# Kernel optimization log

Hardware: AMD Instinct MI355X
Metric: run time of the kernel (lower is better)

## Reference

```python
import jax, jax.numpy as jnp
import numpy as np

B, S, D = 4, 4096, 256
H, K = 4, 64  # num_heads, key_dim
EPS = 1e-3    # Keras LayerNormalization default epsilon
NEG = -1e9    # Keras additive mask constant for float32


def setup_inputs() -> dict:
    key = jax.random.key(0)
    ks = jax.random.split(key, 12)
    sd = 1.0 / np.sqrt(D)
    return {
        "query": jax.random.normal(ks[0], (B, S, D), dtype=jnp.float32),
        "value": jax.random.normal(ks[1], (B, S, D), dtype=jnp.float32),
        "Wq": jax.random.normal(ks[2], (D, H, K), dtype=jnp.float32) * sd,
        "bq": jnp.zeros((H, K), dtype=jnp.float32),
        "Wk": jax.random.normal(ks[3], (D, H, K), dtype=jnp.float32) * sd,
        "bk": jnp.zeros((H, K), dtype=jnp.float32),
        "Wv": jax.random.normal(ks[4], (D, H, K), dtype=jnp.float32) * sd,
        "bv": jnp.zeros((H, K), dtype=jnp.float32),
        "Wo": jax.random.normal(ks[5], (H, K, D), dtype=jnp.float32) * sd,
        "bo": jnp.zeros((D,), dtype=jnp.float32),
        "gamma": jnp.ones((D,), dtype=jnp.float32),
        "beta": jnp.zeros((D,), dtype=jnp.float32),
    }


def reference(query, value, Wq, bq, Wk, bk, Wv, bv, Wo, bo, gamma, beta):
    # Keras MHA(query, value): key defaults to value
    q = jnp.einsum("bsd,dhk->bshk", query, Wq) + bq
    k = jnp.einsum("bsd,dhk->bshk", value, Wk) + bk
    v = jnp.einsum("bsd,dhk->bshk", value, Wv) + bv
    scores = jnp.einsum("bqhk,bshk->bhqs", q, k) / jnp.sqrt(jnp.float32(K))
    # lower-triangular causal mask, applied additively (Keras semantics)
    causal = jnp.tril(jnp.ones((q.shape[1], q.shape[1]), dtype=bool))
    scores = scores + jnp.where(causal, 0.0, NEG)
    attn = jax.nn.softmax(scores, axis=-1)  # [B,H,S,S]
    ctx = jnp.einsum("bhqs,bshk->bqhk", attn, v)
    mha_out = jnp.einsum("bqhk,hkd->bqd", ctx, Wo) + bo
    # residual + LayerNorm (over last axis)
    x = mha_out + query
    mu = jnp.mean(x, axis=-1, keepdims=True)
    var = jnp.mean(jnp.square(x - mu), axis=-1, keepdims=True)
    return (x - mu) * jax.lax.rsqrt(var + EPS) * gamma + beta
```

## Files before the change

kernel.cpp:

```cpp
#include <hip/hip_runtime.h>
#include <hip/hip_bf16.h>
#include <stdint.h>

#define SS 4096
#define DD 256
#define HH 4
#define KK 64
#define ALPHA 0.18033688011112042f

typedef float f32x4 __attribute__((ext_vector_type(4)));
typedef short s16x8 __attribute__((ext_vector_type(8)));
typedef unsigned int u32;

__device__ __forceinline__ unsigned short f2bf(float x) {
  union { float f; unsigned u; } v; v.f = x;
  unsigned r = v.u + 0x7fffu + ((v.u >> 16) & 1u);
  return (unsigned short)(r >> 16);
}

__device__ __forceinline__ u32 cvtpk(float lo, float hi) {
  u32 r;
  asm("v_cvt_pk_bf16_f32 %0, %1, %2" : "=v"(r) : "v"(lo), "v"(hi));
  return r;
}

#define fexp2(x) __builtin_amdgcn_exp2f(x)

__device__ __forceinline__ void gl_lds16(const unsigned short* g, unsigned short* l) {
  __builtin_amdgcn_global_load_lds(
      (const __attribute__((address_space(1))) u32*)g,
      (__attribute__((address_space(3))) u32*)l, 16, 0, 0);
}

__global__ void wprep(const float* __restrict__ Wq, const float* __restrict__ Wk,
                      const float* __restrict__ Wv, const float* __restrict__ Wo,
                      unsigned short* __restrict__ Wt, unsigned short* __restrict__ Wot)
{
  const int blk = blockIdx.x, t = threadIdx.x;
  const int rsub = t >> 4;
  const int c0 = (t & 15) * 16;
  if (blk < 48) {
    const int n = blk * 16 + rsub;
    const float* W = (n < 256) ? Wq : ((n < 512) ? Wk : Wv);
    const int nn = n & 255;
    const float sc = (n < 256) ? ALPHA : 1.0f;
    for (int c = c0; c < c0 + 16; ++c)
      Wt[(size_t)n * 256 + c] = f2bf(sc * W[(size_t)c * 256 + nn]);
  } else {
    const int d = (blk - 48) * 16 + rsub;
    for (int c = c0; c < c0 + 16; ++c)
      Wot[(size_t)d * 256 + c] = f2bf(Wo[(size_t)c * 256 + d]);
  }
}

__global__ __launch_bounds__(256, 3) void qkv_mfma(
    const float* __restrict__ query, const float* __restrict__ value,
    const unsigned short* __restrict__ Wt,
    const float* __restrict__ bq, const float* __restrict__ bk,
    const float* __restrict__ bv,
    unsigned short* __restrict__ qb, unsigned short* __restrict__ kbs,
    unsigned short* __restrict__ vts)
{
  __shared__ __align__(16) unsigned short Xs[64 * 256];

  const int t = threadIdx.x;
  const int w = t >> 6, l = t & 63, lr = l & 15, grp = l >> 4;
  const int mat = (int)(blockIdx.x % 3u);
  const int rb  = (int)(blockIdx.x / 3u);
  const long r0 = (long)rb * 64;

  const float* X = (mat == 0) ? query : value;

  {
    const int row = t >> 2;
    const int c0s = (t & 3) * 64;
    const float* xp = X + (r0 + row) * 256 + c0s;
    const int sw = (row & 7) << 3;
    #pragma unroll
    for (int g = 0; g < 8; ++g) {
      f32x4 x0 = *(const f32x4*)(xp + g * 8);
      f32x4 x1 = *(const f32x4*)(xp + g * 8 + 4);
      union { u32 wd[4]; s16x8 v; } bb;
      bb.wd[0] = cvtpk(x0[0], x0[1]);
      bb.wd[1] = cvtpk(x0[2], x0[3]);
      bb.wd[2] = cvtpk(x1[0], x1[1]);
      bb.wd[3] = cvtpk(x1[2], x1[3]);
      *(s16x8*)&Xs[(row * 256 + c0s + g * 8) ^ sw] = bb.v;
    }
  }
  __syncthreads();

  const int n0 = w * 64;
  const int swr = (lr & 7) << 3;

  f32x4 acc[4][4] = {};

  #pragma unroll 2
  for (int k0 = 0; k0 < 256; k0 += 32) {
    s16x8 xf[4];
    #pragma unroll
    for (int mt = 0; mt < 4; ++mt)
      xf[mt] = *(const s16x8*)&Xs[((mt * 16 + lr) * 256 + k0 + grp * 8) ^ swr];
    #pragma unroll
    for (int nt = 0; nt < 4; ++nt) {
      s16x8 af = *(const s16x8*)(Wt + (size_t)(mat * 256 + n0 + nt * 16 + lr) * 256 + k0 + grp * 8);
      if (mat == 2) {
        #pragma unroll
        for (int mt = 0; mt < 4; ++mt)
          acc[mt][nt] = __builtin_amdgcn_mfma_f32_16x16x32_bf16(xf[mt], af, acc[mt][nt], 0, 0, 0);
      } else {
        #pragma unroll
        for (int mt = 0; mt < 4; ++mt)
          acc[mt][nt] = __builtin_amdgcn_mfma_f32_16x16x32_bf16(af, xf[mt], acc[mt][nt], 0, 0, 0);
      }
    }
  }

  const int b  = (int)(r0 >> 12);
  const int s0 = (int)(r0 & 4095);
  const int kt = s0 >> 6;
  const size_t base = (size_t)(b * 4 + w) * (SS * KK) + (size_t)kt * 4096;

  if (mat == 0) {
    #pragma unroll
    for (int nt = 0; nt < 4; ++nt) {
      const int nk = nt * 16 + grp * 4;
      f32x4 bias = *(const f32x4*)&bq[n0 + nk] * ALPHA;
      #pragma unroll
      for (int mt = 0; mt < 4; ++mt) {
        const int s = s0 + mt * 16 + lr;
        f32x4 o = acc[mt][nt] + bias;
        uint2 pk2; pk2.x = cvtpk(o[0], o[1]); pk2.y = cvtpk(o[2], o[3]);
        *(uint2*)&qb[((size_t)(b * 4 + w) * SS + s) * KK + nk] = pk2;
      }
    }
  } else if (mat == 1) {
    #pragma unroll
    for (int nt = 0; nt < 4; ++nt) {
      const int d0 = nt * 16 + grp * 4;
      const int cc = d0 >> 5, grpk = (d0 >> 3) & 3, jlo = d0 & 7;
      f32x4 bias = *(const f32x4*)&bk[n0 + d0];
      #pragma unroll
      for (int mt = 0; mt < 4; ++mt) {
        const int chunk = ((mt * 2 + cc) * 4 + grpk) * 16 + lr;
        f32x4 o = acc[mt][nt] + bias;
        uint2 pk2; pk2.x = cvtpk(o[0], o[1]); pk2.y = cvtpk(o[2], o[3]);
        *(uint2*)&kbs[base + chunk * 8 + jlo] = pk2;
      }
    }
  } else {
    #pragma unroll
    for (int nt = 0; nt < 4; ++nt) {
      const float bvn = bv[n0 + nt * 16 + lr];
      #pragma unroll
      for (int mt = 0; mt < 4; ++mt) {
        const int cb = (nt * 2 + (mt >> 1)) * 64 + grp * 16 + lr;
        f32x4 o = acc[mt][nt] + bvn;
        uint2 pk2; pk2.x = cvtpk(o[0], o[1]); pk2.y = cvtpk(o[2], o[3]);
        *(uint2*)&vts[base + (size_t)cb * 8 + (mt & 1) * 4] = pk2;
      }
    }
  }
}

__global__ __launch_bounds__(256, 2) void attn(
    const unsigned short* __restrict__ qb,
    const unsigned short* __restrict__ kbs,
    const unsigned short* __restrict__ vts,
    float* __restrict__ num0, float* __restrict__ num1,
    float* __restrict__ lb0, float* __restrict__ lb1)
{
  __shared__ __align__(16) unsigned short Kl[2][4096];
  __shared__ __align__(16) unsigned short Vl[2][4096];

  const int t = threadIdx.x;
  const int w = t >> 6, l = t & 63, lr = l & 15, grp = l >> 4;

  const int i    = blockIdx.x;
  const int bh   = i & 15;
  const int pr   = (i >> 4) & 15;
  const int role = i >> 8;
  const int b = bh >> 2, h = bh & 3;
  const int phA_last = 2 * pr + 1;

  const unsigned short* kbase = kbs + (size_t)bh * (SS * KK);
  const unsigned short* vbase = vts + (size_t)bh * (SS * KK);
  const unsigned short* qpb   = qb  + (size_t)bh * (SS * KK);

  int sup = (role == 0) ? pr : (31 - pr);

  s16x8 qf[2][2];
  #pragma unroll
  for (int q2 = 0; q2 < 2; ++q2) {
    const unsigned short* qp = qpb + (size_t)(sup * 128 + w * 32 + q2 * 16 + lr) * KK;
    qf[q2][0] = *(const s16x8*)(qp + grp * 8);
    qf[q2][1] = *(const s16x8*)(qp + 32 + grp * 8);
  }

  s16x8 ones;
  #pragma unroll
  for (int e = 0; e < 8; ++e) ones[e] = (short)0x3F80;
  const f32x4 minit = {-16.f, -16.f, -16.f, -16.f};

  f32x4 cacc[2][4] = {};
  f32x4 lacc[2] = {};

  const int off0 = (w * 64 + l) * 8;
  const int off1 = ((4 + w) * 64 + l) * 8;

  {
    const int kt0 = (role == 0) ? 0 : (31 - 2 * pr);
    const unsigned short* ks = kbase + (size_t)kt0 * 4096;
    const unsigned short* vs = vbase + (size_t)kt0 * 4096;
    gl_lds16(ks + off0, &Kl[0][w * 512]);
    gl_lds16(ks + off1, &Kl[0][(4 + w) * 512]);
    gl_lds16(vs + off0, &Vl[0][w * 512]);
    gl_lds16(vs + off1, &Vl[0][(4 + w) * 512]);
  }
  __syncthreads();

  for (int ss = 0; ss <= 32; ++ss) {
    const int cur = ss & 1;
    const int kt = (role == 0)
        ? ((ss <= phA_last) ? ss : (ss - (phA_last + 1)))
        : (31 - 2 * pr + ss);

    if (ss < 32) {
      const int ktn = (role == 0)
          ? ((ss + 1 <= phA_last) ? (ss + 1) : (ss + 1 - (phA_last + 1)))
          : (31 - 2 * pr + ss + 1);
      const unsigned short* ks = kbase + (size_t)ktn * 4096;
      const unsigned short* vs = vbase + (size_t)ktn * 4096;
      unsigned short* Kd = &Kl[cur ^ 1][0];
      unsigned short* Vd = &Vl[cur ^ 1][0];
      gl_lds16(ks + off0, Kd + w * 512);
      gl_lds16(ks + off1, Kd + (4 + w) * 512);
      gl_lds16(vs + off0, Vd + w * 512);
      gl_lds16(vs + off1, Vd + (4 + w) * 512);
    }

    if (!(kt == 2 * sup + 1 && w < 2)) {
      const unsigned short* Kb = &Kl[cur][0];
      const unsigned short* Vb = &Vl[cur][0];

      s16x8 kf[8];
      #pragma unroll
      for (int kc = 0; kc < 8; ++kc)
        kf[kc] = *(const s16x8*)&Kb[((kc * 4 + grp) * 16 + lr) * 8];

      f32x4 sc[2][4];
      #pragma unroll
      for (int q2 = 0; q2 < 2; ++q2) {
        #pragma unroll
        for (int kvt = 0; kvt < 4; ++kvt) {
          f32x4 a = __builtin_amdgcn_mfma_f32_16x16x32_bf16(kf[kvt * 2 + 0], qf[q2][0], minit, 0, 0, 0);
          a = __builtin_amdgcn_mfma_f32_16x16x32_bf16(kf[kvt * 2 + 1], qf[q2][1], a, 0, 0, 0);
          sc[q2][kvt] = a;
        }
      }

      if (kt >= 2 * sup) {
        const int kvb0 = kt * 64;
        #pragma unroll
        for (int q2 = 0; q2 < 2; ++q2) {
          const int qrow = sup * 128 + w * 32 + q2 * 16 + lr;
          #pragma unroll
          for (int kvt = 0; kvt < 4; ++kvt)
            #pragma unroll
            for (int e = 0; e < 4; ++e)
              if ((kvb0 + kvt * 16 + grp * 4 + e) > qrow) sc[q2][kvt][e] += -1.0e9f;
        }
      }

      #pragma unroll
      for (int q2 = 0; q2 < 2; ++q2)
        #pragma unroll
        for (int kvt = 0; kvt < 4; ++kvt)
          #pragma unroll
          for (int e = 0; e < 4; ++e)
            sc[q2][kvt][e] = fexp2(sc[q2][kvt][e]);

      s16x8 pf[2][2];
      #pragma unroll
      for (int q2 = 0; q2 < 2; ++q2) {
        #pragma unroll
        for (int kap = 0; kap < 2; ++kap) {
          union { u32 wd[4]; s16x8 v; } pu;
          pu.wd[0] = cvtpk(sc[q2][2 * kap][0], sc[q2][2 * kap][1]);
          pu.wd[1] = cvtpk(sc[q2][2 * kap][2], sc[q2][2 * kap][3]);
          pu.wd[2] = cvtpk(sc[q2][2 * kap + 1][0], sc[q2][2 * kap + 1][1]);
          pu.wd[3] = cvtpk(sc[q2][2 * kap + 1][2], sc[q2][2 * kap + 1][3]);
          pf[q2][kap] = pu.v;
        }
      }

      #pragma unroll
      for (int m2 = 0; m2 < 4; ++m2) {
        #pragma unroll
        for (int kap = 0; kap < 2; ++kap) {
          s16x8 vfr = *(const s16x8*)&Vb[((m2 * 2 + kap) * 64 + l) * 8];
          cacc[0][m2] = __builtin_amdgcn_mfma_f32_16x16x32_bf16(vfr, pf[0][kap], cacc[0][m2], 0, 0, 0);
          cacc[1][m2] = __builtin_amdgcn_mfma_f32_16x16x32_bf16(vfr, pf[1][kap], cacc[1][m2], 0, 0, 0);
        }
      }
      #pragma unroll
      for (int q2 = 0; q2 < 2; ++q2) {
        lacc[q2] = __builtin_amdgcn_mfma_f32_16x16x32_bf16(ones, pf[q2][0], lacc[q2], 0, 0, 0);
        lacc[q2] = __builtin_amdgcn_mfma_f32_16x16x32_bf16(ones, pf[q2][1], lacc[q2], 0, 0, 0);
      }
    }

    if (role == 0 && ss == phA_last) {
      #pragma unroll
      for (int q2 = 0; q2 < 2; ++q2) {
        const int rowg = sup * 128 + w * 32 + q2 * 16 + lr;
        float* np_ = num0 + ((size_t)((b << 12) + rowg)) * 256 + h * 64;
        #pragma unroll
        for (int m2 = 0; m2 < 4; ++m2) {
          *(f32x4*)&np_[m2 * 16 + grp * 4] = cacc[q2][m2];
          cacc[q2][m2] = (f32x4){0.f, 0.f, 0.f, 0.f};
        }
        if (grp == 0) lb0[(bh << 12) + rowg] = lacc[q2][0];
        lacc[q2] = (f32x4){0.f, 0.f, 0.f, 0.f};
      }
      sup = 31 - pr;
      #pragma unroll
      for (int q2 = 0; q2 < 2; ++q2) {
        const unsigned short* qp = qpb + (size_t)(sup * 128 + w * 32 + q2 * 16 + lr) * KK;
        qf[q2][0] = *(const s16x8*)(qp + grp * 8);
        qf[q2][1] = *(const s16x8*)(qp + 32 + grp * 8);
      }
    }
    __syncthreads();
  }

  if (role == 0) {
    #pragma unroll
    for (int q2 = 0; q2 < 2; ++q2) {
      const int rowg = sup * 128 + w * 32 + q2 * 16 + lr;
      float* np_ = num0 + ((size_t)((b << 12) + rowg)) * 256 + h * 64;
      #pragma unroll
      for (int m2 = 0; m2 < 4; ++m2)
        *(f32x4*)&np_[m2 * 16 + grp * 4] = cacc[q2][m2];
      if (grp == 0) lb0[(bh << 12) + rowg] = lacc[q2][0];
    }
  } else {
    #pragma unroll
    for (int q2 = 0; q2 < 2; ++q2) {
      const int rowg = sup * 128 + w * 32 + q2 * 16 + lr;
      float* np_ = num1 + ((size_t)((b << 11) + (rowg - 2048))) * 256 + h * 64;
      #pragma unroll
      for (int m2 = 0; m2 < 4; ++m2)
        *(f32x4*)&np_[m2 * 16 + grp * 4] = cacc[q2][m2];
      if (grp == 0) lb1[(bh << 11) + (rowg - 2048)] = lacc[q2][0];
    }
  }
}

__global__ __launch_bounds__(256, 4) void oproj_ln(
    const float* __restrict__ num0, const float* __restrict__ num1,
    const float* __restrict__ lb0, const float* __restrict__ lb1,
    const unsigned short* __restrict__ Wot,
    const float* __restrict__ bo, const float* __restrict__ query,
    const float* __restrict__ gamma, const float* __restrict__ beta,
    float* __restrict__ out)
{
  __shared__ __align__(16) float redS[32][4];
  __shared__ __align__(16) float redQ[32][4];

  const int t = threadIdx.x;
  const int w = t >> 6, l = t & 63, lr = l & 15, grp = l >> 4;
  const long r0 = (long)blockIdx.x * 32;
  const int n0c = w * 64;
  const int b = (int)(r0 >> 12);
  const bool heavy = ((r0 >> 11) & 1) != 0;

  float invl[2][4];
  #pragma unroll
  for (int mt = 0; mt < 2; ++mt) {
    const int grow = (int)r0 + mt * 16 + lr;
    #pragma unroll
    for (int h = 0; h < 4; ++h) {
      float lv = lb0[((b * 4 + h) << 12) + (grow & 4095)];
      if (heavy) lv += lb1[((b * 4 + h) << 11) + (grow & 2047)];
      invl[mt][h] = 1.0f / lv;
    }
  }

  f32x4 acc[2][4] = {};

  #pragma unroll
  for (int k0 = 0; k0 < 256; k0 += 32) {
    s16x8 bfr[2];
    #pragma unroll
    for (int mt = 0; mt < 2; ++mt) {
      const int grow = (int)r0 + mt * 16 + lr;
      const int c = k0 + grp * 8;
      const float* p0 = num0 + (size_t)grow * 256 + c;
      f32x4 a0 = *(const f32x4*)p0;
      f32x4 a1 = *(const f32x4*)(p0 + 4);
      if (heavy) {
        const float* p1 = num1 + ((size_t)((b << 11) + (grow & 2047))) * 256 + c;
        a0 += *(const f32x4*)p1;
        a1 += *(const f32x4*)(p1 + 4);
      }
      const float iv = invl[mt][k0 >> 6];
      a0 *= iv; a1 *= iv;
      union { u32 wd[4]; s16x8 v; } bb;
      bb.wd[0] = cvtpk(a0[0], a0[1]);
      bb.wd[1] = cvtpk(a0[2], a0[3]);
      bb.wd[2] = cvtpk(a1[0], a1[1]);
      bb.wd[3] = cvtpk(a1[2], a1[3]);
      bfr[mt] = bb.v;
    }
    #pragma unroll
    for (int nt = 0; nt < 4; ++nt) {
      s16x8 af = *(const s16x8*)(Wot + (size_t)(n0c + nt * 16 + lr) * 256 + k0 + grp * 8);
      acc[0][nt] = __builtin_amdgcn_mfma_f32_16x16x32_bf16(af, bfr[0], acc[0][nt], 0, 0, 0);
      acc[1][nt] = __builtin_amdgcn_mfma_f32_16x16x32_bf16(af, bfr[1], acc[1][nt], 0, 0, 0);
    }
  }

  float sm[2] = {0.f, 0.f}, sq[2] = {0.f, 0.f};
  #pragma unroll
  for (int mt = 0; mt < 2; ++mt) {
    const long s = r0 + mt * 16 + lr;
    #pragma unroll
    for (int nt = 0; nt < 4; ++nt) {
      const int n = n0c + nt * 16 + grp * 4;
      f32x4 v = acc[mt][nt] + *(const f32x4*)&bo[n] + *(const f32x4*)&query[s * 256 + n];
      acc[mt][nt] = v;
      sm[mt] += v[0] + v[1] + v[2] + v[3];
      sq[mt] += v[0]*v[0] + v[1]*v[1] + v[2]*v[2] + v[3]*v[3];
    }
    sm[mt] += __shfl_xor(sm[mt], 16); sm[mt] += __shfl_xor(sm[mt], 32);
    sq[mt] += __shfl_xor(sq[mt], 16); sq[mt] += __shfl_xor(sq[mt], 32);
  }
  if (grp == 0) {
    redS[0 * 16 + lr][w] = sm[0]; redQ[0 * 16 + lr][w] = sq[0];
    redS[1 * 16 + lr][w] = sm[1]; redQ[1 * 16 + lr][w] = sq[1];
  }
  __syncthreads();

  #pragma unroll
  for (int mt = 0; mt < 2; ++mt) {
    f32x4 s4 = *(const f32x4*)&redS[mt * 16 + lr][0];
    f32x4 q4 = *(const f32x4*)&redQ[mt * 16 + lr][0];
    const float tot = s4[0] + s4[1] + s4[2] + s4[3];
    const float tq  = q4[0] + q4[1] + q4[2] + q4[3];
    const float mu  = tot * 0.00390625f;
    const float var = tq * 0.00390625f - mu * mu;
    const float rs  = rsqrtf(var + 1.0e-3f);
    const long s = r0 + mt * 16 + lr;
    #pragma unroll
    for (int nt = 0; nt < 4; ++nt) {
      const int n = n0c + nt * 16 + grp * 4;
      f32x4 g = *(const f32x4*)&gamma[n];
      f32x4 bt = *(const f32x4*)&beta[n];
      f32x4 o = (acc[mt][nt] - mu) * rs * g + bt;
      *(f32x4*)&out[s * 256 + n] = o;
    }
  }
}

extern "C" void kernel_launch(void* const* d_in, const int* in_sizes, int n_in,
                              void* d_out, int out_size, void* d_ws, size_t ws_size,
                              hipStream_t stream) {
  const float* query = (const float*)d_in[0];
  const float* value = (const float*)d_in[1];
  const float* Wq    = (const float*)d_in[2];
  const float* bq    = (const float*)d_in[3];
  const float* Wk    = (const float*)d_in[4];
  const float* bk    = (const float*)d_in[5];
  const float* Wv    = (const float*)d_in[6];
  const float* bv    = (const float*)d_in[7];
  const float* Wo    = (const float*)d_in[8];
  const float* bo    = (const float*)d_in[9];
  const float* gamma = (const float*)d_in[10];
  const float* beta  = (const float*)d_in[11];
  float* out = (float*)d_out;

  char* ws = (char*)d_ws;
  unsigned short* qb   = (unsigned short*)ws;
  unsigned short* kbs  = (unsigned short*)(ws + ((size_t)8  << 20));
  unsigned short* vts  = (unsigned short*)(ws + ((size_t)16 << 20));
  float* num0          = (float*)(ws + ((size_t)24 << 20));
  float* num1          = (float*)(ws + ((size_t)40 << 20));
  float* lb0           = (float*)(ws + ((size_t)48 << 20));
  float* lb1           = (float*)(ws + ((size_t)48 << 20) + ((size_t)256 << 10));
  unsigned short* Wt   = (unsigned short*)(ws + ((size_t)48 << 20) + ((size_t)512 << 10));
  unsigned short* Wot  = Wt + (size_t)768 * 256;

  wprep<<<64, 256, 0, stream>>>(Wq, Wk, Wv, Wo, Wt, Wot);
  qkv_mfma<<<768, 256, 0, stream>>>(query, value, Wt, bq, bk, bv, qb, kbs, vts);
  attn<<<512, 256, 0, stream>>>(qb, kbs, vts, num0, num1, lb0, lb1);
  oproj_ln<<<512, 256, 0, stream>>>(num0, num1, lb0, lb1, Wot, bo, query, gamma, beta, out);
}
```

Measured before the change: 109.1 us.

## Fuse QKV projections per row block and triple-buffer K/V staging in attention

The QKV kernel now processes 32 rows per block and computes Q, K and V together from shared LDS tiles of query and value, replacing separate per-matrix blocks of 64 rows. This removes the duplicate load and conversion of value rows for K and V, at the cost of fewer rows reusing each weight load and a lower occupancy bound. The attention kernel moves from double to triple buffering of K/V tiles, staging two tiles ahead and waiting with an explicit vmcnt and raw barriers instead of a full syncthreads. This aims to hide global-to-LDS latency better but uses more LDS and relies on exact vmcnt accounting.

```diff
diff --git a/kernel.cpp b/kernel.cpp
--- a/kernel.cpp
+++ b/kernel.cpp
@@ -53,7 +53,7 @@
   }
 }
 
-__global__ __launch_bounds__(256, 3) void qkv_mfma(
+__global__ __launch_bounds__(256, 2) void qkv_mfma(
     const float* __restrict__ query, const float* __restrict__ value,
     const unsigned short* __restrict__ Wt,
     const float* __restrict__ bq, const float* __restrict__ bk,
@@ -61,31 +61,36 @@
     unsigned short* __restrict__ qb, unsigned short* __restrict__ kbs,
     unsigned short* __restrict__ vts)
 {
-  __shared__ __align__(16) unsigned short Xs[64 * 256];
+  __shared__ __align__(16) unsigned short Xq[32 * 256];
+  __shared__ __align__(16) unsigned short Xv[32 * 256];
 
   const int t = threadIdx.x;
   const int w = t >> 6, l = t & 63, lr = l & 15, grp = l >> 4;
-  const int mat = (int)(blockIdx.x % 3u);
-  const int rb  = (int)(blockIdx.x / 3u);
-  const long r0 = (long)rb * 64;
-
-  const float* X = (mat == 0) ? query : value;
+  const long r0 = (long)blockIdx.x * 32;
 
   {
-    const int row = t >> 2;
-    const int c0s = (t & 3) * 64;
-    const float* xp = X + (r0 + row) * 256 + c0s;
+    const int row = t >> 3;
+    const int c0s = (t & 7) * 32;
     const int sw = (row & 7) << 3;
-    #pragma unroll
-    for (int g = 0; g < 8; ++g) {
-      f32x4 x0 = *(const f32x4*)(xp + g * 8);
-      f32x4 x1 = *(const f32x4*)(xp + g * 8 + 4);
+    const float* qp_ = query + (r0 + row) * 256 + c0s;
+    const float* vp_ = value + (r0 + row) * 256 + c0s;
+    #pragma unroll
+    for (int g = 0; g < 4; ++g) {
+      f32x4 q0 = *(const f32x4*)(qp_ + g * 8);
+      f32x4 q1 = *(const f32x4*)(qp_ + g * 8 + 4);
       union { u32 wd[4]; s16x8 v; } bb;
-      bb.wd[0] = cvtpk(x0[0], x0[1]);
-      bb.wd[1] = cvtpk(x0[2], x0[3]);
-      bb.wd[2] = cvtpk(x1[0], x1[1]);
-      bb.wd[3] = cvtpk(x1[2], x1[3]);
-      *(s16x8*)&Xs[(row * 256 + c0s + g * 8) ^ sw] = bb.v;
+      bb.wd[0] = cvtpk(q0[0], q0[1]);
+      bb.wd[1] = cvtpk(q0[2], q0[3]);
+      bb.wd[2] = cvtpk(q1[0], q1[1]);
+      bb.wd[3] = cvtpk(q1[2], q1[3]);
+      *(s16x8*)&Xq[(row * 256 + c0s + g * 8) ^ sw] = bb.v;
+      f32x4 v0 = *(const f32x4*)(vp_ + g * 8);
+      f32x4 v1 = *(const f32x4*)(vp_ + g * 8 + 4);
+      bb.wd[0] = cvtpk(v0[0], v0[1]);
+      bb.wd[1] = cvtpk(v0[2], v0[3]);
+      bb.wd[2] = cvtpk(v1[0], v1[1]);
+      bb.wd[3] = cvtpk(v1[2], v1[3]);
+      *(s16x8*)&Xv[(row * 256 + c0s + g * 8) ^ sw] = bb.v;
     }
   }
   __syncthreads();
@@ -93,71 +98,75 @@
   const int n0 = w * 64;
   const int swr = (lr & 7) << 3;
 
-  f32x4 acc[4][4] = {};
-
-  #pragma unroll 2
+  f32x4 aq[2][4] = {}, ak[2][4] = {}, av[2][4] = {};
+
   for (int k0 = 0; k0 < 256; k0 += 32) {
-    s16x8 xf[4];
-    #pragma unroll
-    for (int mt = 0; mt < 4; ++mt)
-      xf[mt] = *(const s16x8*)&Xs[((mt * 16 + lr) * 256 + k0 + grp * 8) ^ swr];
+    s16x8 xq[2], xv[2];
+    #pragma unroll
+    for (int mt = 0; mt < 2; ++mt) {
+      const int idx = ((mt * 16 + lr) * 256 + k0 + grp * 8) ^ swr;
+      xq[mt] = *(const s16x8*)&Xq[idx];
+      xv[mt] = *(const s16x8*)&Xv[idx];
+    }
     #pragma unroll
     for (int nt = 0; nt < 4; ++nt) {
-      s16x8 af = *(const s16x8*)(Wt + (size_t)(mat * 256 + n0 + nt * 16 + lr) * 256 + k0 + grp * 8);
-      if (mat == 2) {
-        #pragma unroll
-        for (int mt = 0; mt < 4; ++mt)
-          acc[mt][nt] = __builtin_amdgcn_mfma_f32_16x16x32_bf16(xf[mt], af, acc[mt][nt], 0, 0, 0);
-      } else {
-        #pragma unroll
-        for (int mt = 0; mt < 4; ++mt)
-          acc[mt][nt] = __builtin_amdgcn_mfma_f32_16x16x32_bf16(af, xf[mt], acc[mt][nt], 0, 0, 0);
-      }
-    }
-  }
-
-  const int b  = (int)(r0 >> 12);
-  const int s0 = (int)(r0 & 4095);
-  const int kt = s0 >> 6;
-  const size_t base = (size_t)(b * 4 + w) * (SS * KK) + (size_t)kt * 4096;
-
-  if (mat == 0) {
-    #pragma unroll
-    for (int nt = 0; nt < 4; ++nt) {
-      const int nk = nt * 16 + grp * 4;
-      f32x4 bias = *(const f32x4*)&bq[n0 + nk] * ALPHA;
-      #pragma unroll
-      for (int mt = 0; mt < 4; ++mt) {
-        const int s = s0 + mt * 16 + lr;
-        f32x4 o = acc[mt][nt] + bias;
-        uint2 pk2; pk2.x = cvtpk(o[0], o[1]); pk2.y = cvtpk(o[2], o[3]);
-        *(uint2*)&qb[((size_t)(b * 4 + w) * SS + s) * KK + nk] = pk2;
-      }
-    }
-  } else if (mat == 1) {
-    #pragma unroll
-    for (int nt = 0; nt < 4; ++nt) {
-      const int d0 = nt * 16 + grp * 4;
-      const int cc = d0 >> 5, grpk = (d0 >> 3) & 3, jlo = d0 & 7;
-      f32x4 bias = *(const f32x4*)&bk[n0 + d0];
-      #pragma unroll
-      for (int mt = 0; mt < 4; ++mt) {
-        const int chunk = ((mt * 2 + cc) * 4 + grpk) * 16 + lr;
-        f32x4 o = acc[mt][nt] + bias;
-        uint2 pk2; pk2.x = cvtpk(o[0], o[1]); pk2.y = cvtpk(o[2], o[3]);
-        *(uint2*)&kbs[base + chunk * 8 + jlo] = pk2;
-      }
-    }
-  } else {
+      const size_t wrow = (size_t)(n0 + nt * 16 + lr) * 256 + k0 + grp * 8;
+      s16x8 aQ = *(const s16x8*)(Wt + wrow);
+      s16x8 aK = *(const s16x8*)(Wt + (size_t)256 * 256 + wrow);
+      s16x8 aV = *(const s16x8*)(Wt + (size_t)512 * 256 + wrow);
+      #pragma unroll
+      for (int mt = 0; mt < 2; ++mt) {
+        aq[mt][nt] = __builtin_amdgcn_mfma_f32_16x16x32_bf16(aQ, xq[mt], aq[mt][nt], 0, 0, 0);
+        ak[mt][nt] = __builtin_amdgcn_mfma_f32_16x16x32_bf16(aK, xv[mt], ak[mt][nt], 0, 0, 0);
+        av[mt][nt] = __builtin_amdgcn_mfma_f32_16x16x32_bf16(xv[mt], aV, av[mt][nt], 0, 0, 0);
+      }
+    }
+  }
+
+  const int b   = (int)(r0 >> 12);
+  const int s0  = (int)(r0 & 4095);
+  const int kt  = s0 >> 6;
+  const int kvb = s0 & 63;
+  const int bh  = b * 4 + w;
+  const size_t base = (size_t)bh * (SS * KK) + (size_t)kt * 4096;
+
+  #pragma unroll
+  for (int nt = 0; nt < 4; ++nt) {
+    const int nk = nt * 16 + grp * 4;
+    f32x4 bias = *(const f32x4*)&bq[n0 + nk] * ALPHA;
+    #pragma unroll
+    for (int mt = 0; mt < 2; ++mt) {
+      const int s = s0 + mt * 16 + lr;
+      f32x4 o = aq[mt][nt] + bias;
+      uint2 pk2; pk2.x = cvtpk(o[0], o[1]); pk2.y = cvtpk(o[2], o[3]);
+      *(uint2*)&qb[((size_t)bh * SS + s) * KK + nk] = pk2;
+    }
+  }
+  #pragma unroll
+  for (int nt = 0; nt < 4; ++nt) {
+    const int d0 = nt * 16 + grp * 4;
+    const int cc = d0 >> 5, grpk = (d0 >> 3) & 3, jlo = d0 & 7;
+    f32x4 bias = *(const f32x4*)&bk[n0 + d0];
+    #pragma unroll
+    for (int mt = 0; mt < 2; ++mt) {
+      const int kv = kvb + mt * 16 + lr;
+      const int chunk = (((kv >> 4) * 2 + cc) * 4 + grpk) * 16 + (kv & 15);
+      f32x4 o = ak[mt][nt] + bias;
+      uint2 pk2; pk2.x = cvtpk(o[0], o[1]); pk2.y = cvtpk(o[2], o[3]);
+      *(uint2*)&kbs[base + chunk * 8 + jlo] = pk2;
+    }
+  }
+  {
+    const int kap = (kvb >> 5) & 1;
     #pragma unroll
     for (int nt = 0; nt < 4; ++nt) {
       const float bvn = bv[n0 + nt * 16 + lr];
-      #pragma unroll
-      for (int mt = 0; mt < 4; ++mt) {
-        const int cb = (nt * 2 + (mt >> 1)) * 64 + grp * 16 + lr;
-        f32x4 o = acc[mt][nt] + bvn;
+      const int cb = (nt * 2 + kap) * 64 + grp * 16 + lr;
+      #pragma unroll
+      for (int mt = 0; mt < 2; ++mt) {
+        f32x4 o = av[mt][nt] + bvn;
         uint2 pk2; pk2.x = cvtpk(o[0], o[1]); pk2.y = cvtpk(o[2], o[3]);
-        *(uint2*)&vts[base + (size_t)cb * 8 + (mt & 1) * 4] = pk2;
+        *(uint2*)&vts[base + (size_t)cb * 8 + mt * 4] = pk2;
       }
     }
   }
@@ -170,8 +179,8 @@
     float* __restrict__ num0, float* __restrict__ num1,
     float* __restrict__ lb0, float* __restrict__ lb1)
 {
-  __shared__ __align__(16) unsigned short Kl[2][4096];
-  __shared__ __align__(16) unsigned short Vl[2][4096];
+  __shared__ __align__(16) unsigned short Kl[3][4096];
+  __shared__ __align__(16) unsigned short Vl[3][4096];
 
   const int t = threadIdx.x;
   const int w = t >> 6, l = t & 63, lr = l & 15, grp = l >> 4;
@@ -208,37 +217,32 @@
   const int off0 = (w * 64 + l) * 8;
   const int off1 = ((4 + w) * 64 + l) * 8;
 
-  {
-    const int kt0 = (role == 0) ? 0 : (31 - 2 * pr);
-    const unsigned short* ks = kbase + (size_t)kt0 * 4096;
-    const unsigned short* vs = vbase + (size_t)kt0 * 4096;
-    gl_lds16(ks + off0, &Kl[0][w * 512]);
-    gl_lds16(ks + off1, &Kl[0][(4 + w) * 512]);
-    gl_lds16(vs + off0, &Vl[0][w * 512]);
-    gl_lds16(vs + off1, &Vl[0][(4 + w) * 512]);
-  }
-  __syncthreads();
+  auto ktfor = [&](int s) {
+    if (s > 32) s = 32;
+    return (role == 0) ? ((s <= phA_last) ? s : (s - (phA_last + 1)))
+                       : (31 - 2 * pr + s);
+  };
+  auto stage = [&](int kt, int bi) {
+    const unsigned short* ks = kbase + (size_t)kt * 4096;
+    const unsigned short* vs = vbase + (size_t)kt * 4096;
+    gl_lds16(ks + off0, &Kl[bi][w * 512]);
+    gl_lds16(ks + off1, &Kl[bi][(4 + w) * 512]);
+    gl_lds16(vs + off0, &Vl[bi][w * 512]);
+    gl_lds16(vs + off1, &Vl[bi][(4 + w) * 512]);
+  };
+
+  stage(ktfor(0), 0);
+  stage(ktfor(1), 1);
 
   for (int ss = 0; ss <= 32; ++ss) {
-    const int cur = ss & 1;
-    const int kt = (role == 0)
-        ? ((ss <= phA_last) ? ss : (ss - (phA_last + 1)))
-        : (31 - 2 * pr + ss);
-
-    if (ss < 32) {
-      const int ktn = (role == 0)
-          ? ((ss + 1 <= phA_last) ? (ss + 1) : (ss + 1 - (phA_last + 1)))
-          : (31 - 2 * pr + ss + 1);
-      const unsigned short* ks = kbase + (size_t)ktn * 4096;
-      const unsigned short* vs = vbase + (size_t)ktn * 4096;
-      unsigned short* Kd = &Kl[cur ^ 1][0];
-      unsigned short* Vd = &Vl[cur ^ 1][0];
-      gl_lds16(ks + off0, Kd + w * 512);
-      gl_lds16(ks + off1, Kd + (4 + w) * 512);
-      gl_lds16(vs + off0, Vd + w * 512);
-      gl_lds16(vs + off1, Vd + (4 + w) * 512);
-    }
-
+    const int cur = ss % 3;
+    stage(ktfor(ss + 2), (ss + 2) % 3);
+
+    asm volatile("s_waitcnt vmcnt(8)" ::: "memory");
+    __builtin_amdgcn_s_barrier();
+    __builtin_amdgcn_sched_barrier(0);
+
+    const int kt = ktfor(ss);
     if (!(kt == 2 * sup + 1 && w < 2)) {
       const unsigned short* Kb = &Kl[cur][0];
       const unsigned short* Vb = &Vl[cur][0];
@@ -331,7 +335,9 @@
         qf[q2][1] = *(const s16x8*)(qp + 32 + grp * 8);
       }
     }
-    __syncthreads();
+
+    __builtin_amdgcn_sched_barrier(0);
+    __builtin_amdgcn_s_barrier();
   }
 
   if (role == 0) {
@@ -492,7 +498,7 @@
   unsigned short* Wot  = Wt + (size_t)768 * 256;
 
   wprep<<<64, 256, 0, stream>>>(Wq, Wk, Wv, Wo, Wt, Wot);
-  qkv_mfma<<<768, 256, 0, stream>>>(query, value, Wt, bq, bk, bv, qb, kbs, vts);
+  qkv_mfma<<<512, 256, 0, stream>>>(query, value, Wt, bq, bk, bv, qb, kbs, vts);
   attn<<<512, 256, 0, stream>>>(qb, kbs, vts, num0, num1, lb0, lb1);
   oproj_ln<<<512, 256, 0, stream>>>(num0, num1, lb0, lb1, Wot, bo, query, gamma, beta, out);
 }
```

Result: slower. 116.7 us (+6.9%).

## Split attention into 64-row query tiles with per-wave KV halves and bf16 partials

Applied to the files above, without the earlier changes.

The attention kernel now uses 64-row query tiles instead of 128 and launches 1024 blocks with a higher occupancy hint. Each pair of waves splits every 64-key tile into two 32-key halves, so each wave writes its own partial numerator and denominator buffer. Partials are stored as bf16 rather than fp32, and the output-projection kernel sums up to four partial buffers. The aims are better load balance and occupancy, no idle masked waves on the diagonal, and less partial-result traffic. In exchange it adds precision loss in the partials and extra reduction reads in the projection kernel.

```diff
diff --git a/kernel.cpp b/kernel.cpp
--- a/kernel.cpp
+++ b/kernel.cpp
@@ -30,6 +30,15 @@
   __builtin_amdgcn_global_load_lds(
       (const __attribute__((address_space(1))) u32*)g,
       (__attribute__((address_space(3))) u32*)l, 16, 0, 0);
+}
+
+__device__ __forceinline__ void acc8(const unsigned short* p, f32x4& a0, f32x4& a1) {
+  s16x8 v = *(const s16x8*)p;
+  union { u32 u; float f; } c;
+  #pragma unroll
+  for (int j = 0; j < 4; ++j) { c.u = ((u32)(unsigned short)v[j]) << 16; a0[j] += c.f; }
+  #pragma unroll
+  for (int j = 0; j < 4; ++j) { c.u = ((u32)(unsigned short)v[4 + j]) << 16; a1[j] += c.f; }
 }
 
 __global__ void wprep(const float* __restrict__ Wq, const float* __restrict__ Wk,
@@ -163,36 +172,39 @@
   }
 }
 
-__global__ __launch_bounds__(256, 2) void attn(
+__global__ __launch_bounds__(256, 4) void attn(
     const unsigned short* __restrict__ qb,
     const unsigned short* __restrict__ kbs,
     const unsigned short* __restrict__ vts,
-    float* __restrict__ num0, float* __restrict__ num1,
-    float* __restrict__ lb0, float* __restrict__ lb1)
+    unsigned short* __restrict__ ns0, unsigned short* __restrict__ ns1,
+    unsigned short* __restrict__ ns2, unsigned short* __restrict__ ns3,
+    float* __restrict__ lb0, float* __restrict__ lb1,
+    float* __restrict__ lb2, float* __restrict__ lb3)
 {
   __shared__ __align__(16) unsigned short Kl[2][4096];
   __shared__ __align__(16) unsigned short Vl[2][4096];
 
   const int t = threadIdx.x;
   const int w = t >> 6, l = t & 63, lr = l & 15, grp = l >> 4;
+  const int qg = w >> 1, kh = w & 1;
 
   const int i    = blockIdx.x;
   const int bh   = i & 15;
-  const int pr   = (i >> 4) & 15;
-  const int role = i >> 8;
+  const int pr   = (i >> 4) & 31;
+  const int role = (i >> 9) & 1;
   const int b = bh >> 2, h = bh & 3;
-  const int phA_last = 2 * pr + 1;
 
   const unsigned short* kbase = kbs + (size_t)bh * (SS * KK);
   const unsigned short* vbase = vts + (size_t)bh * (SS * KK);
   const unsigned short* qpb   = qb  + (size_t)bh * (SS * KK);
 
-  int sup = (role == 0) ? pr : (31 - pr);
+  int sup = (role == 0) ? pr : (63 - pr);
+  const int nsteps = 33 - role;
 
   s16x8 qf[2][2];
   #pragma unroll
   for (int q2 = 0; q2 < 2; ++q2) {
-    const unsigned short* qp = qpb + (size_t)(sup * 128 + w * 32 + q2 * 16 + lr) * KK;
+    const unsigned short* qp = qpb + (size_t)(sup * 64 + qg * 32 + q2 * 16 + lr) * KK;
     qf[q2][0] = *(const s16x8*)(qp + grp * 8);
     qf[q2][1] = *(const s16x8*)(qp + 32 + grp * 8);
   }
@@ -208,125 +220,106 @@
   const int off0 = (w * 64 + l) * 8;
   const int off1 = ((4 + w) * 64 + l) * 8;
 
-  {
-    const int kt0 = (role == 0) ? 0 : (31 - 2 * pr);
-    const unsigned short* ks = kbase + (size_t)kt0 * 4096;
-    const unsigned short* vs = vbase + (size_t)kt0 * 4096;
-    gl_lds16(ks + off0, &Kl[0][w * 512]);
-    gl_lds16(ks + off1, &Kl[0][(4 + w) * 512]);
-    gl_lds16(vs + off0, &Vl[0][w * 512]);
-    gl_lds16(vs + off1, &Vl[0][(4 + w) * 512]);
-  }
+  auto ktfor = [&](int s) {
+    return (role == 0) ? ((s <= pr) ? s : (s - (pr + 1))) : (32 - pr + s);
+  };
+  auto stage = [&](int kt, int bi) {
+    const unsigned short* ks = kbase + (size_t)kt * 4096;
+    const unsigned short* vs = vbase + (size_t)kt * 4096;
+    gl_lds16(ks + off0, &Kl[bi][w * 512]);
+    gl_lds16(ks + off1, &Kl[bi][(4 + w) * 512]);
+    gl_lds16(vs + off0, &Vl[bi][w * 512]);
+    gl_lds16(vs + off1, &Vl[bi][(4 + w) * 512]);
+  };
+
+  stage(ktfor(0), 0);
   __syncthreads();
 
-  for (int ss = 0; ss <= 32; ++ss) {
+  for (int ss = 0; ss < nsteps; ++ss) {
     const int cur = ss & 1;
-    const int kt = (role == 0)
-        ? ((ss <= phA_last) ? ss : (ss - (phA_last + 1)))
-        : (31 - 2 * pr + ss);
-
-    if (ss < 32) {
-      const int ktn = (role == 0)
-          ? ((ss + 1 <= phA_last) ? (ss + 1) : (ss + 1 - (phA_last + 1)))
-          : (31 - 2 * pr + ss + 1);
-      const unsigned short* ks = kbase + (size_t)ktn * 4096;
-      const unsigned short* vs = vbase + (size_t)ktn * 4096;
-      unsigned short* Kd = &Kl[cur ^ 1][0];
-      unsigned short* Vd = &Vl[cur ^ 1][0];
-      gl_lds16(ks + off0, Kd + w * 512);
-      gl_lds16(ks + off1, Kd + (4 + w) * 512);
-      gl_lds16(vs + off0, Vd + w * 512);
-      gl_lds16(vs + off1, Vd + (4 + w) * 512);
-    }
-
-    if (!(kt == 2 * sup + 1 && w < 2)) {
-      const unsigned short* Kb = &Kl[cur][0];
-      const unsigned short* Vb = &Vl[cur][0];
-
-      s16x8 kf[8];
-      #pragma unroll
-      for (int kc = 0; kc < 8; ++kc)
-        kf[kc] = *(const s16x8*)&Kb[((kc * 4 + grp) * 16 + lr) * 8];
-
-      f32x4 sc[2][4];
+    if (ss + 1 < nsteps) stage(ktfor(ss + 1), cur ^ 1);
+
+    const int kt = ktfor(ss);
+    const unsigned short* Kb = &Kl[cur][0];
+    const unsigned short* Vb = &Vl[cur][0];
+
+    s16x8 kf[4];
+    #pragma unroll
+    for (int j = 0; j < 4; ++j)
+      kf[j] = *(const s16x8*)&Kb[(((kh * 4 + j) * 4 + grp) * 16 + lr) * 8];
+
+    f32x4 sc[2][2];
+    #pragma unroll
+    for (int q2 = 0; q2 < 2; ++q2) {
+      #pragma unroll
+      for (int tt = 0; tt < 2; ++tt) {
+        f32x4 a = __builtin_amdgcn_mfma_f32_16x16x32_bf16(kf[tt * 2 + 0], qf[q2][0], minit, 0, 0, 0);
+        a = __builtin_amdgcn_mfma_f32_16x16x32_bf16(kf[tt * 2 + 1], qf[q2][1], a, 0, 0, 0);
+        sc[q2][tt] = a;
+      }
+    }
+
+    if (kt == sup) {
       #pragma unroll
       for (int q2 = 0; q2 < 2; ++q2) {
+        const int qloc = qg * 32 + q2 * 16 + lr;
         #pragma unroll
-        for (int kvt = 0; kvt < 4; ++kvt) {
-          f32x4 a = __builtin_amdgcn_mfma_f32_16x16x32_bf16(kf[kvt * 2 + 0], qf[q2][0], minit, 0, 0, 0);
-          a = __builtin_amdgcn_mfma_f32_16x16x32_bf16(kf[kvt * 2 + 1], qf[q2][1], a, 0, 0, 0);
-          sc[q2][kvt] = a;
-        }
-      }
-
-      if (kt >= 2 * sup) {
-        const int kvb0 = kt * 64;
-        #pragma unroll
-        for (int q2 = 0; q2 < 2; ++q2) {
-          const int qrow = sup * 128 + w * 32 + q2 * 16 + lr;
-          #pragma unroll
-          for (int kvt = 0; kvt < 4; ++kvt)
-            #pragma unroll
-            for (int e = 0; e < 4; ++e)
-              if ((kvb0 + kvt * 16 + grp * 4 + e) > qrow) sc[q2][kvt][e] += -1.0e9f;
-        }
-      }
-
-      #pragma unroll
-      for (int q2 = 0; q2 < 2; ++q2)
-        #pragma unroll
-        for (int kvt = 0; kvt < 4; ++kvt)
+        for (int tt = 0; tt < 2; ++tt)
           #pragma unroll
           for (int e = 0; e < 4; ++e)
-            sc[q2][kvt][e] = fexp2(sc[q2][kvt][e]);
-
-      s16x8 pf[2][2];
+            if (((kh * 2 + tt) * 16 + grp * 4 + e) > qloc) sc[q2][tt][e] += -1.0e9f;
+      }
+    }
+
+    #pragma unroll
+    for (int q2 = 0; q2 < 2; ++q2)
+      #pragma unroll
+      for (int tt = 0; tt < 2; ++tt)
+        #pragma unroll
+        for (int e = 0; e < 4; ++e)
+          sc[q2][tt][e] = fexp2(sc[q2][tt][e]);
+
+    s16x8 pf[2];
+    #pragma unroll
+    for (int q2 = 0; q2 < 2; ++q2) {
+      union { u32 wd[4]; s16x8 v; } pu;
+      pu.wd[0] = cvtpk(sc[q2][0][0], sc[q2][0][1]);
+      pu.wd[1] = cvtpk(sc[q2][0][2], sc[q2][0][3]);
+      pu.wd[2] = cvtpk(sc[q2][1][0], sc[q2][1][1]);
+      pu.wd[3] = cvtpk(sc[q2][1][2], sc[q2][1][3]);
+      pf[q2] = pu.v;
+    }
+
+    #pragma unroll
+    for (int m2 = 0; m2 < 4; ++m2) {
+      s16x8 vfr = *(const s16x8*)&Vb[((m2 * 2 + kh) * 64 + l) * 8];
+      cacc[0][m2] = __builtin_amdgcn_mfma_f32_16x16x32_bf16(vfr, pf[0], cacc[0][m2], 0, 0, 0);
+      cacc[1][m2] = __builtin_amdgcn_mfma_f32_16x16x32_bf16(vfr, pf[1], cacc[1][m2], 0, 0, 0);
+    }
+    lacc[0] = __builtin_amdgcn_mfma_f32_16x16x32_bf16(ones, pf[0], lacc[0], 0, 0, 0);
+    lacc[1] = __builtin_amdgcn_mfma_f32_16x16x32_bf16(ones, pf[1], lacc[1], 0, 0, 0);
+
+    if (role == 0 && ss == pr) {
+      unsigned short* nsl = kh ? ns1 : ns0;
+      float* lbl = kh ? lb1 : lb0;
       #pragma unroll
       for (int q2 = 0; q2 < 2; ++q2) {
-        #pragma unroll
-        for (int kap = 0; kap < 2; ++kap) {
-          union { u32 wd[4]; s16x8 v; } pu;
-          pu.wd[0] = cvtpk(sc[q2][2 * kap][0], sc[q2][2 * kap][1]);
-          pu.wd[1] = cvtpk(sc[q2][2 * kap][2], sc[q2][2 * kap][3]);
-          pu.wd[2] = cvtpk(sc[q2][2 * kap + 1][0], sc[q2][2 * kap + 1][1]);
-          pu.wd[3] = cvtpk(sc[q2][2 * kap + 1][2], sc[q2][2 * kap + 1][3]);
-          pf[q2][kap] = pu.v;
-        }
-      }
-
-      #pragma unroll
-      for (int m2 = 0; m2 < 4; ++m2) {
-        #pragma unroll
-        for (int kap = 0; kap < 2; ++kap) {
-          s16x8 vfr = *(const s16x8*)&Vb[((m2 * 2 + kap) * 64 + l) * 8];
-          cacc[0][m2] = __builtin_amdgcn_mfma_f32_16x16x32_bf16(vfr, pf[0][kap], cacc[0][m2], 0, 0, 0);
-          cacc[1][m2] = __builtin_amdgcn_mfma_f32_16x16x32_bf16(vfr, pf[1][kap], cacc[1][m2], 0, 0, 0);
-        }
-      }
-      #pragma unroll
-      for (int q2 = 0; q2 < 2; ++q2) {
-        lacc[q2] = __builtin_amdgcn_mfma_f32_16x16x32_bf16(ones, pf[q2][0], lacc[q2], 0, 0, 0);
-        lacc[q2] = __builtin_amdgcn_mfma_f32_16x16x32_bf16(ones, pf[q2][1], lacc[q2], 0, 0, 0);
-      }
-    }
-
-    if (role == 0 && ss == phA_last) {
-      #pragma unroll
-      for (int q2 = 0; q2 < 2; ++q2) {
-        const int rowg = sup * 128 + w * 32 + q2 * 16 + lr;
-        float* np_ = num0 + ((size_t)((b << 12) + rowg)) * 256 + h * 64;
+        const int rowg = sup * 64 + qg * 32 + q2 * 16 + lr;
+        unsigned short* np_ = nsl + ((size_t)((b << 12) + rowg)) * 256 + h * 64;
         #pragma unroll
         for (int m2 = 0; m2 < 4; ++m2) {
-          *(f32x4*)&np_[m2 * 16 + grp * 4] = cacc[q2][m2];
+          uint2 pk2; pk2.x = cvtpk(cacc[q2][m2][0], cacc[q2][m2][1]);
+          pk2.y = cvtpk(cacc[q2][m2][2], cacc[q2][m2][3]);
+          *(uint2*)&np_[m2 * 16 + grp * 4] = pk2;
           cacc[q2][m2] = (f32x4){0.f, 0.f, 0.f, 0.f};
         }
-        if (grp == 0) lb0[(bh << 12) + rowg] = lacc[q2][0];
+        if (grp == 0) lbl[(bh << 12) + rowg] = lacc[q2][0];
         lacc[q2] = (f32x4){0.f, 0.f, 0.f, 0.f};
       }
-      sup = 31 - pr;
+      sup = 63 - pr;
       #pragma unroll
       for (int q2 = 0; q2 < 2; ++q2) {
-        const unsigned short* qp = qpb + (size_t)(sup * 128 + w * 32 + q2 * 16 + lr) * KK;
+        const unsigned short* qp = qpb + (size_t)(sup * 64 + qg * 32 + q2 * 16 + lr) * KK;
         qf[q2][0] = *(const s16x8*)(qp + grp * 8);
         qf[q2][1] = *(const s16x8*)(qp + 32 + grp * 8);
       }
@@ -335,31 +328,43 @@
   }
 
   if (role == 0) {
+    unsigned short* nsl = kh ? ns1 : ns0;
+    float* lbl = kh ? lb1 : lb0;
     #pragma unroll
     for (int q2 = 0; q2 < 2; ++q2) {
-      const int rowg = sup * 128 + w * 32 + q2 * 16 + lr;
-      float* np_ = num0 + ((size_t)((b << 12) + rowg)) * 256 + h * 64;
-      #pragma unroll
-      for (int m2 = 0; m2 < 4; ++m2)
-        *(f32x4*)&np_[m2 * 16 + grp * 4] = cacc[q2][m2];
-      if (grp == 0) lb0[(bh << 12) + rowg] = lacc[q2][0];
+      const int rowg = sup * 64 + qg * 32 + q2 * 16 + lr;
+      unsigned short* np_ = nsl + ((size_t)((b << 12) + rowg)) * 256 + h * 64;
+      #pragma unroll
+      for (int m2 = 0; m2 < 4; ++m2) {
+        uint2 pk2; pk2.x = cvtpk(cacc[q2][m2][0], cacc[q2][m2][1]);
+        pk2.y = cvtpk(cacc[q2][m2][2], cacc[q2][m2][3]);
+        *(uint2*)&np_[m2 * 16 + grp * 4] = pk2;
+      }
+      if (grp == 0) lbl[(bh << 12) + rowg] = lacc[q2][0];
     }
   } else {
+    unsigned short* nsl = kh ? ns3 : ns2;
+    float* lbl = kh ? lb3 : lb2;
     #pragma unroll
     for (int q2 = 0; q2 < 2; ++q2) {
-      const int rowg = sup * 128 + w * 32 + q2 * 16 + lr;
-      float* np_ = num1 + ((size_t)((b << 11) + (rowg - 2048))) * 256 + h * 64;
-      #pragma unroll
-      for (int m2 = 0; m2 < 4; ++m2)
-        *(f32x4*)&np_[m2 * 16 + grp * 4] = cacc[q2][m2];
-      if (grp == 0) lb1[(bh << 11) + (rowg - 2048)] = lacc[q2][0];
+      const int rowg = sup * 64 + qg * 32 + q2 * 16 + lr;
+      unsigned short* np_ = nsl + ((size_t)((b << 11) + (rowg - 2048))) * 256 + h * 64;
+      #pragma unroll
+      for (int m2 = 0; m2 < 4; ++m2) {
+        uint2 pk2; pk2.x = cvtpk(cacc[q2][m2][0], cacc[q2][m2][1]);
+        pk2.y = cvtpk(cacc[q2][m2][2], cacc[q2][m2][3]);
+        *(uint2*)&np_[m2 * 16 + grp * 4] = pk2;
+      }
+      if (grp == 0) lbl[(bh << 11) + (rowg - 2048)] = lacc[q2][0];
     }
   }
 }
 
 __global__ __launch_bounds__(256, 4) void oproj_ln(
-    const float* __restrict__ num0, const float* __restrict__ num1,
+    const unsigned short* __restrict__ ns0, const unsigned short* __restrict__ ns1,
+    const unsigned short* __restrict__ ns2, const unsigned short* __restrict__ ns3,
     const float* __restrict__ lb0, const float* __restrict__ lb1,
+    const float* __restrict__ lb2, const float* __restrict__ lb3,
     const unsigned short* __restrict__ Wot,
     const float* __restrict__ bo, const float* __restrict__ query,
     const float* __restrict__ gamma, const float* __restrict__ beta,
@@ -381,8 +386,12 @@
     const int grow = (int)r0 + mt * 16 + lr;
     #pragma unroll
     for (int h = 0; h < 4; ++h) {
-      float lv = lb0[((b * 4 + h) << 12) + (grow & 4095)];
-      if (heavy) lv += lb1[((b * 4 + h) << 11) + (grow & 2047)];
+      const int i12 = ((b * 4 + h) << 12) + (grow & 4095);
+      float lv = lb0[i12] + lb1[i12];
+      if (heavy) {
+        const int i11 = ((b * 4 + h) << 11) + (grow & 2047);
+        lv += lb2[i11] + lb3[i11];
+      }
       invl[mt][h] = 1.0f / lv;
     }
   }
@@ -396,13 +405,14 @@
     for (int mt = 0; mt < 2; ++mt) {
       const int grow = (int)r0 + mt * 16 + lr;
       const int c = k0 + grp * 8;
-      const float* p0 = num0 + (size_t)grow * 256 + c;
-      f32x4 a0 = *(const f32x4*)p0;
-      f32x4 a1 = *(const f32x4*)(p0 + 4);
+      f32x4 a0 = {0.f, 0.f, 0.f, 0.f}, a1 = {0.f, 0.f, 0.f, 0.f};
+      const size_t o01 = (size_t)grow * 256 + c;
+      acc8(ns0 + o01, a0, a1);
+      acc8(ns1 + o01, a0, a1);
       if (heavy) {
-        const float* p1 = num1 + ((size_t)((b << 11) + (grow & 2047))) * 256 + c;
-        a0 += *(const f32x4*)p1;
-        a1 += *(const f32x4*)(p1 + 4);
+        const size_t o23 = ((size_t)((b << 11) + (grow & 2047))) * 256 + c;
+        acc8(ns2 + o23, a0, a1);
+        acc8(ns3 + o23, a0, a1);
       }
       const float iv = invl[mt][k0 >> 6];
       a0 *= iv; a1 *= iv;
@@ -481,18 +491,23 @@
   float* out = (float*)d_out;
 
   char* ws = (char*)d_ws;
-  unsigned short* qb   = (unsigned short*)ws;
-  unsigned short* kbs  = (unsigned short*)(ws + ((size_t)8  << 20));
-  unsigned short* vts  = (unsigned short*)(ws + ((size_t)16 << 20));
-  float* num0          = (float*)(ws + ((size_t)24 << 20));
-  float* num1          = (float*)(ws + ((size_t)40 << 20));
-  float* lb0           = (float*)(ws + ((size_t)48 << 20));
-  float* lb1           = (float*)(ws + ((size_t)48 << 20) + ((size_t)256 << 10));
-  unsigned short* Wt   = (unsigned short*)(ws + ((size_t)48 << 20) + ((size_t)512 << 10));
-  unsigned short* Wot  = Wt + (size_t)768 * 256;
+  unsigned short* qb  = (unsigned short*)ws;
+  unsigned short* kbs = (unsigned short*)(ws + ((size_t)8  << 20));
+  unsigned short* vts = (unsigned short*)(ws + ((size_t)16 << 20));
+  unsigned short* ns0 = (unsigned short*)(ws + ((size_t)24 << 20));
+  unsigned short* ns1 = (unsigned short*)(ws + ((size_t)32 << 20));
+  unsigned short* ns2 = (unsigned short*)(ws + ((size_t)40 << 20));
+  unsigned short* ns3 = (unsigned short*)(ws + ((size_t)44 << 20));
+  float* lb0 = (float*)(ws + ((size_t)48 << 20));
+  float* lb1 = (float*)(ws + ((size_t)48 << 20) + ((size_t)256 << 10));
+  float* lb2 = (float*)(ws + ((size_t)48 << 20) + ((size_t)512 << 10));
+  float* lb3 = (float*)(ws + ((size_t)48 << 20) + ((size_t)640 << 10));
+  unsigned short* Wt  = (unsigned short*)(ws + ((size_t)48 << 20) + ((size_t)768 << 10));
+  unsigned short* Wot = Wt + (size_t)768 * 256;
 
   wprep<<<64, 256, 0, stream>>>(Wq, Wk, Wv, Wo, Wt, Wot);
   qkv_mfma<<<768, 256, 0, stream>>>(query, value, Wt, bq, bk, bv, qb, kbs, vts);
-  attn<<<512, 256, 0, stream>>>(qb, kbs, vts, num0, num1, lb0, lb1);
-  oproj_ln<<<512, 256, 0, stream>>>(num0, num1, lb0, lb1, Wot, bo, query, gamma, beta, out);
-}
+  attn<<<1024, 256, 0, stream>>>(qb, kbs, vts, ns0, ns1, ns2, ns3, lb0, lb1, lb2, lb3);
+  oproj_ln<<<512, 256, 0, stream>>>(ns0, ns1, ns2, ns3, lb0, lb1, lb2, lb3,
+                                    Wot, bo, query, gamma, beta, out);
+}
```

After: 110.6 us. About the same (+1.3%).
